# Kernel tuning notes

Hardware: AMD Instinct MI355X
Metric: run time of the kernel (lower is better)

Reference implementation:

```python
import jax, jax.numpy as jnp
import numpy as np

EPS = 1e-5
GROUPS = 8


def setup_inputs() -> dict:
    key = jax.random.key(0)
    ks = jax.random.split(key, 4)
    b, c, h, w = 2, 64, 80, 80
    std = 0.02
    return {
        "x": jax.random.normal(ks[0], (b, c, h, w), dtype=jnp.float32),
        "g_w": jax.random.normal(ks[1], (c, c), dtype=jnp.float32) * std,
        "g_b": jnp.zeros((c,), dtype=jnp.float32),
        "w_w": jax.random.normal(ks[2], (c, c), dtype=jnp.float32) * std,
        "w_b": jnp.zeros((c,), dtype=jnp.float32),
        "gn_w": jax.random.normal(ks[3], (c,), dtype=jnp.float32) * std + 1.0,
        "gn_b": jnp.zeros((c,), dtype=jnp.float32),
    }


def reference(x, g_w, g_b, w_w, w_b, gn_w, gn_b):
    b, c, h, w = x.shape
    n = h * w
    xf = x.reshape(b, c, n)                                   # (b,c,N)
    # g: 1x1 conv -> (b,N,Ci) after permute
    g_x = jnp.einsum('ic,bcn->bni', g_w, xf) + g_b            # (b,N,Ci)
    # theta == phi == flattened x (inter_channels == in_channels)
    aff = jnp.einsum('bcn,bcm->bnm', xf, xf)                  # (b,N,N)
    score = jax.nn.sigmoid(aff)                               # (b,N,N)
    emb = jnp.einsum('bnm,bmi->bni', score, g_x)              # (b,N,Ci)
    emb = emb.transpose(0, 2, 1).reshape(b, c, h, w)          # (b,Ci,h,w)
    # W: 1x1 conv + GroupNorm(8, C)
    y = jnp.einsum('oc,bchw->bohw', w_w, emb) + w_b[None, :, None, None]
    yg = y.reshape(b, GROUPS, c // GROUPS, h, w)
    mean = yg.mean(axis=(2, 3, 4), keepdims=True)
    var = yg.var(axis=(2, 3, 4), keepdims=True)
    yn = ((yg - mean) / jnp.sqrt(var + EPS)).reshape(b, c, h, w)
    out = yn * gn_w[None, :, None, None] + gn_b[None, :, None, None]
    return (out, score)
```

## Files before the change

### kernel.cpp

```cpp
#include <hip/hip_runtime.h>
#include <cstddef>

namespace {
constexpr int B = 2;
constexpr int C = 64;
constexpr int N = 6400;
constexpr int NT = N / 64;
constexpr int MSPLIT = 5;
constexpr int MT_PER = NT / MSPLIT;
constexpr float EPS = 1e-5f;
constexpr int LS = 68;
constexpr int LSB = 72;
}

typedef __attribute__((ext_vector_type(8))) short short8;
typedef __attribute__((ext_vector_type(4))) float f32x4;
typedef __attribute__((ext_vector_type(4))) unsigned short us4v;
typedef __attribute__((ext_vector_type(8))) unsigned short us8v;

__device__ inline unsigned short f2bf(float f) {
  unsigned int u = __float_as_uint(f);
  u += 0x7fffu + ((u >> 16) & 1u);
  return (unsigned short)(u >> 16);
}
__device__ inline float bf2f(unsigned short u) {
  return __uint_as_float(((unsigned int)u) << 16);
}

__global__ __launch_bounds__(256) void xprep_kernel(
    const float* __restrict__ x, const float* __restrict__ g_w,
    const float* __restrict__ g_b, unsigned short* __restrict__ xT,
    unsigned short* __restrict__ gxT) {
  __shared__ float xs[64 * LS];
  __shared__ float gwt[64 * LS];
  const int b = blockIdx.x / NT;
  const int n0 = (blockIdx.x % NT) * 64;
  const int tid = threadIdx.x;
  const int col = tid & 63, row4 = tid >> 6;
  const float* xb = x + (size_t)b * C * N;
#pragma unroll
  for (int it = 0; it < 16; ++it) {
    int r = row4 + it * 4;
    xs[r * LS + col] = xb[(size_t)r * N + n0 + col];
    gwt[col * LS + r] = g_w[r * 64 + col];
  }
  __syncthreads();

  {
    const int ty = tid >> 4, tx = tid & 15;
    float acc[4][4];
#pragma unroll
    for (int a = 0; a < 4; ++a) {
      float gbv = g_b[ty * 4 + a];
      acc[a][0] = gbv; acc[a][1] = gbv; acc[a][2] = gbv; acc[a][3] = gbv;
    }
#pragma unroll 8
    for (int c = 0; c < 64; ++c) {
      const f32x4 a4 = *(const f32x4*)&gwt[c * LS + ty * 4];
      const f32x4 b4 = *(const f32x4*)&xs[c * LS + tx * 4];
#pragma unroll
      for (int a = 0; a < 4; ++a) {
        acc[a][0] += a4[a] * b4[0]; acc[a][1] += a4[a] * b4[1];
        acc[a][2] += a4[a] * b4[2]; acc[a][3] += a4[a] * b4[3];
      }
    }
    unsigned short* gxTb = gxT + (size_t)b * 64 * N;
#pragma unroll
    for (int a = 0; a < 4; ++a) {
      us4v v;
      v[0] = f2bf(acc[a][0]); v[1] = f2bf(acc[a][1]);
      v[2] = f2bf(acc[a][2]); v[3] = f2bf(acc[a][3]);
      *(us4v*)&gxTb[(size_t)(ty * 4 + a) * N + n0 + tx * 4] = v;
    }
  }

  {
    const int nloc = tid >> 2, cs = (tid & 3) * 16;
    us8v u0, u1;
#pragma unroll
    for (int j = 0; j < 8; ++j) u0[j] = f2bf(xs[(cs + j) * LS + nloc]);
#pragma unroll
    for (int j = 0; j < 8; ++j) u1[j] = f2bf(xs[(cs + 8 + j) * LS + nloc]);
    unsigned short* xTb = xT + (size_t)b * N * 64;
    *(us8v*)&xTb[(size_t)(n0 + nloc) * 64 + cs] = u0;
    *(us8v*)&xTb[(size_t)(n0 + nloc) * 64 + cs + 8] = u1;
  }
}

__global__ __launch_bounds__(256, 4) void relation_main(
    const unsigned short* __restrict__ xT, const unsigned short* __restrict__ gxT,
    float* __restrict__ score, float* __restrict__ emb_p) {
  __shared__ alignas(16) unsigned short xnT[64 * LSB];
  __shared__ alignas(16) unsigned short xmT[64 * LSB];
  __shared__ alignas(16) unsigned short gxt[64 * LSB];
  __shared__ alignas(16) unsigned short sc[64 * LSB];

  const int tid = threadIdx.x;
  const int w = tid >> 6, lane = tid & 63;
  const int l15 = lane & 15, quad = lane >> 4;

  const int bIdx = blockIdx.x / (NT * MSPLIT);
  const int rest = blockIdx.x % (NT * MSPLIT);
  const int nt = rest / MSPLIT;
  const int ms = rest % MSPLIT;
  const int n0 = nt * 64;

  const unsigned short* xTb = xT + (size_t)bIdx * N * 64;
  const unsigned short* gxTb = gxT + (size_t)bIdx * 64 * N;
  float* scoreb = score + (size_t)bIdx * N * N;

#pragma unroll
  for (int k = 0; k < 2; ++k) {
    int ch = tid + k * 256;
    int row = ch >> 3, co = (ch & 7) * 8;
    *(us8v*)&xnT[row * LSB + co] = *(const us8v*)&xTb[(size_t)(n0 + row) * 64 + co];
  }

  f32x4 e[4];
  const f32x4 zero = {0.f, 0.f, 0.f, 0.f};
#pragma unroll
  for (int is = 0; is < 4; ++is) e[is] = zero;

  for (int j = 0; j < MT_PER; ++j) {
    const int m0 = (ms * MT_PER + j) * 64;
    __syncthreads();
#pragma unroll
    for (int k = 0; k < 2; ++k) {
      int ch = tid + k * 256;
      int row = ch >> 3, co = (ch & 7) * 8;
      *(us8v*)&xmT[row * LSB + co] = *(const us8v*)&xTb[(size_t)(m0 + row) * 64 + co];
      *(us8v*)&gxt[row * LSB + co] = *(const us8v*)&gxTb[(size_t)row * N + m0 + co];
    }
    __syncthreads();

    short8 a0 = *(const short8*)&xnT[(16 * w + l15) * LSB + 0 * 32 + quad * 8];
    short8 a1 = *(const short8*)&xnT[(16 * w + l15) * LSB + 1 * 32 + quad * 8];
    f32x4 s[4];
#pragma unroll
    for (int msub = 0; msub < 4; ++msub) {
      short8 b0 = *(const short8*)&xmT[(16 * msub + l15) * LSB + 0 * 32 + quad * 8];
      short8 b1 = *(const short8*)&xmT[(16 * msub + l15) * LSB + 1 * 32 + quad * 8];
      f32x4 d = __builtin_amdgcn_mfma_f32_16x16x32_bf16(a0, b0, zero, 0, 0, 0);
      s[msub] = __builtin_amdgcn_mfma_f32_16x16x32_bf16(a1, b1, d, 0, 0, 0);
    }

#pragma unroll
    for (int msub = 0; msub < 4; ++msub) {
#pragma unroll
      for (int r = 0; r < 4; ++r) {
        float t = __builtin_amdgcn_exp2f(-1.442695041f * s[msub][r]);
        float sig = __builtin_amdgcn_rcpf(1.f + t);
        sc[(16 * w + quad * 4 + r) * LSB + 16 * msub + l15] = f2bf(sig);
      }
    }

    short8 p0 = *(const short8*)&sc[(16 * w + l15) * LSB + 0 * 32 + quad * 8];
    short8 p1 = *(const short8*)&sc[(16 * w + l15) * LSB + 1 * 32 + quad * 8];
#pragma unroll
    for (int is = 0; is < 4; ++is) {
      short8 g0 = *(const short8*)&gxt[(16 * is + l15) * LSB + 0 * 32 + quad * 8];
      short8 g1 = *(const short8*)&gxt[(16 * is + l15) * LSB + 1 * 32 + quad * 8];
      e[is] = __builtin_amdgcn_mfma_f32_16x16x32_bf16(p0, g0, e[is], 0, 0, 0);
      e[is] = __builtin_amdgcn_mfma_f32_16x16x32_bf16(p1, g1, e[is], 0, 0, 0);
    }

    __syncthreads();

    {
      const int srow = tid >> 2, scg = (tid & 3) * 16;
      us8v u0 = *(const us8v*)&sc[srow * LSB + scg];
      us8v u1 = *(const us8v*)&sc[srow * LSB + scg + 8];
      float* sp = scoreb + (size_t)(n0 + srow) * N + m0 + scg;
      f32x4 v;
      v[0] = bf2f(u0[0]); v[1] = bf2f(u0[1]); v[2] = bf2f(u0[2]); v[3] = bf2f(u0[3]);
      *(f32x4*)&sp[0] = v;
      v[0] = bf2f(u0[4]); v[1] = bf2f(u0[5]); v[2] = bf2f(u0[6]); v[3] = bf2f(u0[7]);
      *(f32x4*)&sp[4] = v;
      v[0] = bf2f(u1[0]); v[1] = bf2f(u1[1]); v[2] = bf2f(u1[2]); v[3] = bf2f(u1[3]);
      *(f32x4*)&sp[8] = v;
      v[0] = bf2f(u1[4]); v[1] = bf2f(u1[5]); v[2] = bf2f(u1[6]); v[3] = bf2f(u1[7]);
      *(f32x4*)&sp[12] = v;
    }
  }

  float* ep = emb_p + ((size_t)ms * B + bIdx) * (size_t)N * 64;
#pragma unroll
  for (int is = 0; is < 4; ++is) {
#pragma unroll
    for (int r = 0; r < 4; ++r) {
      ep[(size_t)(n0 + 16 * w + quad * 4 + r) * 64 + 16 * is + l15] = e[is][r];
    }
  }
}

__global__ __launch_bounds__(256) void y_kernel(
    const float* __restrict__ emb_p, const float* __restrict__ w_w,
    const float* __restrict__ w_b, float* __restrict__ y) {
  __shared__ float embT[64 * LS];
  __shared__ float wt[64 * LS];
  const int b = blockIdx.x / NT;
  const int n0 = (blockIdx.x % NT) * 64;
  const int tid = threadIdx.x;
  const int col = tid & 63, row4 = tid >> 6;
  const int ty = tid >> 4, tx = tid & 15;
#pragma unroll
  for (int it = 0; it < 16; ++it) {
    int r = row4 + it * 4;
    wt[col * LS + r] = w_w[r * 64 + col];
    float v = 0.f;
#pragma unroll
    for (int msv = 0; msv < MSPLIT; ++msv)
      v += emb_p[((size_t)msv * B + b) * N * C + (size_t)(n0 + r) * C + col];
    embT[col * LS + r] = v;
  }
  __syncthreads();
  float acc[4][4];
#pragma unroll
  for (int a = 0; a < 4; ++a) {
    float wbv = w_b[ty * 4 + a];
    acc[a][0] = wbv; acc[a][1] = wbv; acc[a][2] = wbv; acc[a][3] = wbv;
  }
#pragma unroll 8
  for (int i = 0; i < 64; ++i) {
    const f32x4 w4 = *(const f32x4*)&wt[i * LS + ty * 4];
    const f32x4 e4 = *(const f32x4*)&embT[i * LS + tx * 4];
#pragma unroll
    for (int a = 0; a < 4; ++a) {
      acc[a][0] += w4[a] * e4[0]; acc[a][1] += w4[a] * e4[1];
      acc[a][2] += w4[a] * e4[2]; acc[a][3] += w4[a] * e4[3];
    }
  }
  float* yb = y + (size_t)b * C * N;
#pragma unroll
  for (int a = 0; a < 4; ++a) {
    f32x4 v = {acc[a][0], acc[a][1], acc[a][2], acc[a][3]};
    *(f32x4*)&yb[(size_t)(ty * 4 + a) * N + n0 + tx * 4] = v;
  }
}

__global__ __launch_bounds__(256) void stats_kernel(const float* __restrict__ y,
                                                    float* __restrict__ stats) {
  const int bg = blockIdx.x;
  const f32x4* p = (const f32x4*)(y + (size_t)bg * 8 * N);
  float s = 0.f, q = 0.f;
  for (int i = threadIdx.x; i < 8 * N / 4; i += 256) {
    f32x4 v = p[i];
    s += v[0] + v[1] + v[2] + v[3];
    q += v[0] * v[0] + v[1] * v[1] + v[2] * v[2] + v[3] * v[3];
  }
#pragma unroll
  for (int off = 32; off > 0; off >>= 1) {
    s += __shfl_down(s, off, 64);
    q += __shfl_down(q, off, 64);
  }
  __shared__ float ls[4], lq[4];
  const int lane = threadIdx.x & 63, wv = threadIdx.x >> 6;
  if (lane == 0) { ls[wv] = s; lq[wv] = q; }
  __syncthreads();
  if (threadIdx.x == 0) {
    float S = ls[0] + ls[1] + ls[2] + ls[3];
    float Q = lq[0] + lq[1] + lq[2] + lq[3];
    const float inv = 1.f / (float)(8 * N);
    float mean = S * inv;
    float var = Q * inv - mean * mean;
    stats[bg * 2 + 0] = mean;
    stats[bg * 2 + 1] = rsqrtf(var + EPS);
  }
}

__global__ __launch_bounds__(256) void norm_kernel(
    const float* __restrict__ y, const float* __restrict__ stats,
    const float* __restrict__ gn_w, const float* __restrict__ gn_b,
    float* __restrict__ out) {
  const int idx = blockIdx.x * 256 + threadIdx.x;
  const int e0 = idx * 4;
  const int b = e0 / (C * N);
  const int c = (e0 / N) & 63;
  const int g = c >> 3;
  const float mean = stats[(b * 8 + g) * 2 + 0];
  const float rstd = stats[(b * 8 + g) * 2 + 1];
  const float w = gn_w[c] * rstd;
  const float bb = gn_b[c] - mean * w;
  f32x4 v = *(const f32x4*)&y[e0];
  v[0] = v[0] * w + bb; v[1] = v[1] * w + bb;
  v[2] = v[2] * w + bb; v[3] = v[3] * w + bb;
  *(f32x4*)&out[e0] = v;
}

extern "C" void kernel_launch(void* const* d_in, const int* in_sizes, int n_in,
                              void* d_out, int out_size, void* d_ws, size_t ws_size,
                              hipStream_t stream) {
  const float* x    = (const float*)d_in[0];
  const float* g_w  = (const float*)d_in[1];
  const float* g_b  = (const float*)d_in[2];
  const float* w_w  = (const float*)d_in[3];
  const float* w_b  = (const float*)d_in[4];
  const float* gn_w = (const float*)d_in[5];
  const float* gn_b = (const float*)d_in[6];
  (void)in_sizes; (void)n_in; (void)out_size; (void)ws_size;

  float* out   = (float*)d_out;
  float* score = out + (size_t)B * C * N;

  float* ws    = (float*)d_ws;
  float* emb_p = ws;
  float* y     = emb_p + (size_t)MSPLIT * B * N * C;
  float* stats = y + (size_t)B * C * N;
  unsigned short* xT  = (unsigned short*)(stats + 32);
  unsigned short* gxT = xT + (size_t)B * N * 64;

  hipLaunchKernelGGL(xprep_kernel, dim3(B * NT), dim3(256), 0, stream,
                     x, g_w, g_b, xT, gxT);
  hipLaunchKernelGGL(relation_main, dim3(B * NT * MSPLIT), dim3(256), 0, stream,
                     xT, gxT, score, emb_p);
  hipLaunchKernelGGL(y_kernel, dim3(B * NT), dim3(256), 0, stream, emb_p, w_w, w_b, y);
  hipLaunchKernelGGL(stats_kernel, dim3(B * 8), dim3(256), 0, stream, y, stats);
  hipLaunchKernelGGL(norm_kernel, dim3((B * C * N) / 1024), dim3(256), 0, stream,
                     y, stats, gn_w, gn_b, out);
}
```

Baseline: 435.1 us.

## Prefetch next tile into registers and store score directly from MFMA results

The next m-tile of x and g_x is now loaded into registers while the current tile is computed, a software-pipelined prefetch. The fixed n-tile A operand stays in registers for the whole loop instead of being staged through LDS. Score values are written to global memory as fp32 straight from the sigmoid, which drops the LDS round trip, the bf16 re-read and one block barrier per iteration. The trade-off is narrower, strided 4-byte global stores in place of 16-byte vector stores, plus higher register pressure.

```diff
diff --git a/kernel.cpp b/kernel.cpp
--- a/kernel.cpp
+++ b/kernel.cpp
@@ -90,7 +90,6 @@
 __global__ __launch_bounds__(256, 4) void relation_main(
     const unsigned short* __restrict__ xT, const unsigned short* __restrict__ gxT,
     float* __restrict__ score, float* __restrict__ emb_p) {
-  __shared__ alignas(16) unsigned short xnT[64 * LSB];
   __shared__ alignas(16) unsigned short xmT[64 * LSB];
   __shared__ alignas(16) unsigned short gxt[64 * LSB];
   __shared__ alignas(16) unsigned short sc[64 * LSB];
@@ -109,12 +108,16 @@
   const unsigned short* gxTb = gxT + (size_t)bIdx * 64 * N;
   float* scoreb = score + (size_t)bIdx * N * N;
 
-#pragma unroll
-  for (int k = 0; k < 2; ++k) {
-    int ch = tid + k * 256;
-    int row = ch >> 3, co = (ch & 7) * 8;
-    *(us8v*)&xnT[row * LSB + co] = *(const us8v*)&xTb[(size_t)(n0 + row) * 64 + co];
-  }
+  const short8 a0 = *(const short8*)&xTb[(size_t)(n0 + 16 * w + l15) * 64 + quad * 8];
+  const short8 a1 = *(const short8*)&xTb[(size_t)(n0 + 16 * w + l15) * 64 + 32 + quad * 8];
+
+  const int srow = tid >> 3, sco = (tid & 7) * 8;
+
+  const int mbase = ms * MT_PER * 64;
+  us8v xm0 = *(const us8v*)&xTb[(size_t)(mbase + srow) * 64 + sco];
+  us8v xm1 = *(const us8v*)&xTb[(size_t)(mbase + srow + 32) * 64 + sco];
+  us8v gx0 = *(const us8v*)&gxTb[(size_t)srow * N + mbase + sco];
+  us8v gx1 = *(const us8v*)&gxTb[(size_t)(srow + 32) * N + mbase + sco];
 
   f32x4 e[4];
   const f32x4 zero = {0.f, 0.f, 0.f, 0.f};
@@ -122,28 +125,31 @@
   for (int is = 0; is < 4; ++is) e[is] = zero;
 
   for (int j = 0; j < MT_PER; ++j) {
-    const int m0 = (ms * MT_PER + j) * 64;
+    const int mj = (ms * MT_PER + j) * 64;
     __syncthreads();
-#pragma unroll
-    for (int k = 0; k < 2; ++k) {
-      int ch = tid + k * 256;
-      int row = ch >> 3, co = (ch & 7) * 8;
-      *(us8v*)&xmT[row * LSB + co] = *(const us8v*)&xTb[(size_t)(m0 + row) * 64 + co];
-      *(us8v*)&gxt[row * LSB + co] = *(const us8v*)&gxTb[(size_t)row * N + m0 + co];
-    }
+    *(us8v*)&xmT[srow * LSB + sco] = xm0;
+    *(us8v*)&xmT[(srow + 32) * LSB + sco] = xm1;
+    *(us8v*)&gxt[srow * LSB + sco] = gx0;
+    *(us8v*)&gxt[(srow + 32) * LSB + sco] = gx1;
     __syncthreads();
-
-    short8 a0 = *(const short8*)&xnT[(16 * w + l15) * LSB + 0 * 32 + quad * 8];
-    short8 a1 = *(const short8*)&xnT[(16 * w + l15) * LSB + 1 * 32 + quad * 8];
+    if (j + 1 < MT_PER) {
+      const int m1 = mj + 64;
+      xm0 = *(const us8v*)&xTb[(size_t)(m1 + srow) * 64 + sco];
+      xm1 = *(const us8v*)&xTb[(size_t)(m1 + srow + 32) * 64 + sco];
+      gx0 = *(const us8v*)&gxTb[(size_t)srow * N + m1 + sco];
+      gx1 = *(const us8v*)&gxTb[(size_t)(srow + 32) * N + m1 + sco];
+    }
+
     f32x4 s[4];
 #pragma unroll
     for (int msub = 0; msub < 4; ++msub) {
-      short8 b0 = *(const short8*)&xmT[(16 * msub + l15) * LSB + 0 * 32 + quad * 8];
-      short8 b1 = *(const short8*)&xmT[(16 * msub + l15) * LSB + 1 * 32 + quad * 8];
+      short8 b0 = *(const short8*)&xmT[(16 * msub + l15) * LSB + quad * 8];
+      short8 b1 = *(const short8*)&xmT[(16 * msub + l15) * LSB + 32 + quad * 8];
       f32x4 d = __builtin_amdgcn_mfma_f32_16x16x32_bf16(a0, b0, zero, 0, 0, 0);
       s[msub] = __builtin_amdgcn_mfma_f32_16x16x32_bf16(a1, b1, d, 0, 0, 0);
     }
 
+    float* sp = scoreb + (size_t)(n0 + 16 * w + quad * 4) * N + mj + l15;
 #pragma unroll
     for (int msub = 0; msub < 4; ++msub) {
 #pragma unroll
@@ -151,35 +157,18 @@
         float t = __builtin_amdgcn_exp2f(-1.442695041f * s[msub][r]);
         float sig = __builtin_amdgcn_rcpf(1.f + t);
         sc[(16 * w + quad * 4 + r) * LSB + 16 * msub + l15] = f2bf(sig);
+        sp[(size_t)r * N + 16 * msub] = sig;
       }
     }
 
-    short8 p0 = *(const short8*)&sc[(16 * w + l15) * LSB + 0 * 32 + quad * 8];
-    short8 p1 = *(const short8*)&sc[(16 * w + l15) * LSB + 1 * 32 + quad * 8];
+    short8 p0 = *(const short8*)&sc[(16 * w + l15) * LSB + quad * 8];
+    short8 p1 = *(const short8*)&sc[(16 * w + l15) * LSB + 32 + quad * 8];
 #pragma unroll
     for (int is = 0; is < 4; ++is) {
-      short8 g0 = *(const short8*)&gxt[(16 * is + l15) * LSB + 0 * 32 + quad * 8];
-      short8 g1 = *(const short8*)&gxt[(16 * is + l15) * LSB + 1 * 32 + quad * 8];
+      short8 g0 = *(const short8*)&gxt[(16 * is + l15) * LSB + quad * 8];
+      short8 g1 = *(const short8*)&gxt[(16 * is + l15) * LSB + 32 + quad * 8];
       e[is] = __builtin_amdgcn_mfma_f32_16x16x32_bf16(p0, g0, e[is], 0, 0, 0);
       e[is] = __builtin_amdgcn_mfma_f32_16x16x32_bf16(p1, g1, e[is], 0, 0, 0);
-    }
-
-    __syncthreads();
-
-    {
-      const int srow = tid >> 2, scg = (tid & 3) * 16;
-      us8v u0 = *(const us8v*)&sc[srow * LSB + scg];
-      us8v u1 = *(const us8v*)&sc[srow * LSB + scg + 8];
-      float* sp = scoreb + (size_t)(n0 + srow) * N + m0 + scg;
-      f32x4 v;
-      v[0] = bf2f(u0[0]); v[1] = bf2f(u0[1]); v[2] = bf2f(u0[2]); v[3] = bf2f(u0[3]);
-      *(f32x4*)&sp[0] = v;
-      v[0] = bf2f(u0[4]); v[1] = bf2f(u0[5]); v[2] = bf2f(u0[6]); v[3] = bf2f(u0[7]);
-      *(f32x4*)&sp[4] = v;
-      v[0] = bf2f(u1[0]); v[1] = bf2f(u1[1]); v[2] = bf2f(u1[2]); v[3] = bf2f(u1[3]);
-      *(f32x4*)&sp[8] = v;
-      v[0] = bf2f(u1[4]); v[1] = bf2f(u1[5]); v[2] = bf2f(u1[6]); v[3] = bf2f(u1[7]);
-      *(f32x4*)&sp[12] = v;
     }
   }
 
```

After: 398.0 us. 8.5% less time.
